# Optimization experiments

Measured on AMD Instinct MI355X. Metric: run time of the kernel, lower is better.

The kernel has to match this reference:

```python
import jax, jax.numpy as jnp
import numpy as np

B, N, D = 4, 4096, 256


def setup_inputs() -> dict:
    key = jax.random.key(0)
    k1, k2 = jax.random.split(key)
    val = jax.random.normal(k1, (B, N, D), dtype=jnp.float32)
    state = jax.random.normal(k2, (B, N), dtype=jnp.float32)
    return {"val": val, "state": state}


def reference(val, state):
    # pairwise_fn: scaled dot-product -> scores [B, N, N]
    scale = val.shape[-1] ** -0.5
    scores = jnp.einsum("bid,bjd->bij", val, val) * scale
    # edge_compress_fn = softsign (non-softmax compression)
    edges = scores / (1.0 + jnp.abs(scores))
    # state_weight_edges=False, val/state projections are Identity
    delta_state = jnp.einsum("bij,bj->bi", edges, state)   # [B, N]
    delta_val = jnp.einsum("bij,bjd->bid", edges, val)      # [B, N, D]
    return (delta_state, delta_val)
```

## Files before the change

### kernel.cpp

```cpp
#include <hip/hip_runtime.h>


#define B_  4
#define N_  4096
#define D_  256

typedef __attribute__((ext_vector_type(8))) short short8;
typedef __attribute__((ext_vector_type(4))) float floatx4;

__device__ __forceinline__ unsigned short f2bf(float f) {
    unsigned int u = __float_as_uint(f);
    u += 0x7fff + ((u >> 16) & 1);
    return (unsigned short)(u >> 16);
}

__device__ __forceinline__ void gl_lds16(const void* g, void* l) {
    __builtin_amdgcn_global_load_lds(
        (const __attribute__((address_space(1))) unsigned int*)g,
        (__attribute__((address_space(3))) unsigned int*)l, 16, 0, 0);
}
__device__ __forceinline__ void gl_lds4(const void* g, void* l) {
    __builtin_amdgcn_global_load_lds(
        (const __attribute__((address_space(1))) unsigned int*)g,
        (__attribute__((address_space(3))) unsigned int*)l, 4, 0, 0);
}

__global__ __launch_bounds__(256)
void prepass_kernel(const float* __restrict__ val,
                    unsigned short* __restrict__ Vb,
                    unsigned short* __restrict__ VF) {
    __shared__ unsigned short tile[64][68];
    const int t   = threadIdx.x;
    const int blk = blockIdx.x;
    const int b   = blk >> 8;
    const int it  = (blk >> 2) & 63;
    const int dt  = blk & 3;
    const int i0  = it * 64, d0 = dt * 64;
    const float*    vb  = val + (size_t)b * N_ * D_;
    unsigned short* Vbb = Vb  + (size_t)b * N_ * D_;
    unsigned short* VFb = VF  + (size_t)b * N_ * D_;

    #pragma unroll
    for (int q = 0; q < 4; ++q) {
        int idx = t + 256 * q;
        int row = idx >> 4;
        int c4  = idx & 15;
        float4 v = *(const float4*)(vb + (size_t)(i0 + row) * D_ + d0 + c4 * 4);
        ushort4 h;
        h.x = f2bf(v.x); h.y = f2bf(v.y); h.z = f2bf(v.z); h.w = f2bf(v.w);
        *(ushort4*)(Vbb + (size_t)(i0 + row) * D_ + d0 + c4 * 4) = h;
        *(ushort4*)&tile[row][c4 * 4] = h;
    }
    __syncthreads();
    #pragma unroll
    for (int q = 0; q < 4; ++q) {
        int dr = (t >> 4) + q * 16;
        int i4 = t & 15;
        ushort4 h;
        h.x = tile[i4 * 4 + 0][dr];
        h.y = tile[i4 * 4 + 1][dr];
        h.z = tile[i4 * 4 + 2][dr];
        h.w = tile[i4 * 4 + 3][dr];
        const int jb = (i0 >> 5) + (i4 >> 3);
        const int e  = (i4 & 7) * 4;
        *(ushort4*)(VFb + ((size_t)jb * 256 + d0 + dr) * 32 + e) = h;
    }
}

__global__ __launch_bounds__(512, 1)
void prop_main(const float* __restrict__ state,
               const unsigned short* __restrict__ Vb,
               const unsigned short* __restrict__ VF,
               float* __restrict__ dvp,
               float* __restrict__ dsp_o)
{
    __shared__ __attribute__((aligned(16))) unsigned char smem[103936];

    const int t    = threadIdx.x;
    const int g    = t >> 8;
    const int w    = t >> 6;
    const int w4   = w & 3;
    const int lane = t & 63;
    const int quad = lane >> 4;
    const int l16  = lane & 15;

    const int x   = blockIdx.x;
    const int it  = x >> 3;
    const int b   = (x >> 1) & 3;
    const int jh  = x & 1;
    const int it0 = it * 128;
    const int jbase = jh * 2048;
    const int niter = 32;

    float* dsredg = (float*)(smem + 102912 + g * 512);

    const unsigned short* Vbb = Vb + (size_t)b * N_ * D_;
    const unsigned short* VFb = VF + (size_t)b * N_ * D_;
    const float*          stb = state + (size_t)b * N_;

    const int hi  = lane >> 5;
    const int p32 = lane & 31;

    int vgoff[4];
    #pragma unroll
    for (int n = 0; n < 4; ++n) {
        int r  = 2 * (w * 4 + n) + hi;
        int gr = p32 ^ (r & 7);
        vgoff[n] = r * 256 + gr * 8;
    }

    const int r0 = (w4 >> 1) * 32;
    const int c0 = (w4 & 1) * 32;
    const int pA = l16 & 7;

    const unsigned short* vf_lane = VFb + (size_t)jh * (64 * 8192)
                                  + w4 * 2048 + l16 * 32 + quad * 8;

    short8 A0[8], A1[8];
    {
        const unsigned short* ar0 = Vbb + (size_t)(it0 + g * 64 + r0 + l16) * 256 + quad * 8;
        const unsigned short* ar1 = ar0 + 16 * 256;
        #pragma unroll
        for (int ks = 0; ks < 8; ++ks) {
            A0[ks] = *(const short8*)(ar0 + ks * 32);
            A1[ks] = *(const short8*)(ar1 + ks * 32);
        }
    }

    #pragma unroll
    for (int n = 0; n < 4; ++n)
        gl_lds16(Vbb + (size_t)jbase * 256 + vgoff[n],
                 smem + (w * 4 + n) * 1024);
    if (w == 0) gl_lds4(stb + jbase + lane, smem + 102400);

    floatx4 dv[4][4];
    #pragma unroll
    for (int a = 0; a < 4; ++a)
        #pragma unroll
        for (int c = 0; c < 4; ++c)
            dv[a][c] = (floatx4){0.f, 0.f, 0.f, 0.f};
    float dsp[8];
    #pragma unroll
    for (int k = 0; k < 8; ++k) dsp[k] = 0.f;

    for (int k = 0; k < niter; ++k) {
        const int buf = k & 1;
        unsigned short* Eshg = (unsigned short*)(smem + 65536 + g * 18432 + buf * 9216);
        unsigned short* vjL  = (unsigned short*)(smem + buf * 32768);
        const float*    stj  = (const float*)(smem + 102400 + buf * 256);

        __syncthreads();

        if (k + 1 < niter) {
            const size_t j0n = jbase + (size_t)(k + 1) * 64;
            #pragma unroll
            for (int n = 0; n < 4; ++n)
                gl_lds16(Vbb + j0n * 256 + vgoff[n],
                         smem + (buf ^ 1) * 32768 + (w * 4 + n) * 1024);
            if (w == 0) gl_lds4(stb + j0n + lane, smem + 102400 + (buf ^ 1) * 256);
        }

        short8 bfr[2][4];
        {
            const unsigned short* vfk = vf_lane + (size_t)k * 16384;
            #pragma unroll
            for (int ks = 0; ks < 2; ++ks)
                #pragma unroll
                for (int c2 = 0; c2 < 4; ++c2)
                    bfr[ks][c2] = *(const short8*)(vfk + ks * 8192 + c2 * 512);
        }

        floatx4 sa[2][2];
        #pragma unroll
        for (int a = 0; a < 2; ++a)
            #pragma unroll
            for (int c = 0; c < 2; ++c)
                sa[a][c] = (floatx4){0.f, 0.f, 0.f, 0.f};

        #pragma unroll
        for (int ks = 0; ks < 8; ++ks) {
            const int p = ((ks * 4 + quad) ^ pA) * 8;
            short8 b0 = *(const short8*)&vjL[(c0 + l16) * 256 + p];
            short8 b1 = *(const short8*)&vjL[(c0 + 16 + l16) * 256 + p];
            sa[0][0] = __builtin_amdgcn_mfma_f32_16x16x32_bf16(A0[ks], b0, sa[0][0], 0, 0, 0);
            sa[0][1] = __builtin_amdgcn_mfma_f32_16x16x32_bf16(A0[ks], b1, sa[0][1], 0, 0, 0);
            sa[1][0] = __builtin_amdgcn_mfma_f32_16x16x32_bf16(A1[ks], b0, sa[1][0], 0, 0, 0);
            sa[1][1] = __builtin_amdgcn_mfma_f32_16x16x32_bf16(A1[ks], b1, sa[1][1], 0, 0, 0);
        }

        float stc0 = stj[c0 + l16];
        float stc1 = stj[c0 + 16 + l16];
        #pragma unroll
        for (int a = 0; a < 2; ++a) {
            #pragma unroll
            for (int r = 0; r < 4; ++r) {
                const int il = r0 + a * 16 + quad * 4 + r;
                float s0 = sa[a][0][r];
                float s1 = sa[a][1][r];
                float e0 = s0 * __builtin_amdgcn_rcpf(16.0f + fabsf(s0));
                float e1 = s1 * __builtin_amdgcn_rcpf(16.0f + fabsf(s1));
                dsp[a * 4 + r] += e0 * stc0 + e1 * stc1;
                Eshg[il * 72 + c0 + l16]      = f2bf(e0);
                Eshg[il * 72 + c0 + 16 + l16] = f2bf(e1);
            }
        }
        __syncthreads();

        #pragma unroll
        for (int ks = 0; ks < 2; ++ks) {
            short8 af[4];
            #pragma unroll
            for (int a2 = 0; a2 < 4; ++a2)
                af[a2] = *(const short8*)&Eshg[(a2 * 16 + l16) * 72 + ks * 32 + quad * 8];
            #pragma unroll
            for (int a2 = 0; a2 < 4; ++a2)
                #pragma unroll
                for (int c2 = 0; c2 < 4; ++c2)
                    dv[a2][c2] = __builtin_amdgcn_mfma_f32_16x16x32_bf16(af[a2], bfr[ks][c2], dv[a2][c2], 0, 0, 0);
        }
    }

    float* dvo = dvp + (size_t)jh * B_ * N_ * D_ + (size_t)b * N_ * D_
                     + (size_t)(it0 + g * 64) * D_;
    #pragma unroll
    for (int a2 = 0; a2 < 4; ++a2)
        #pragma unroll
        for (int c2 = 0; c2 < 4; ++c2)
            #pragma unroll
            for (int r = 0; r < 4; ++r) {
                const int il = a2 * 16 + quad * 4 + r;
                const int d  = w4 * 64 + c2 * 16 + l16;
                dvo[(size_t)il * D_ + d] = dv[a2][c2][r];
            }

    #pragma unroll
    for (int k = 0; k < 8; ++k) {
        float v = dsp[k];
        v += __shfl_xor(v, 1);
        v += __shfl_xor(v, 2);
        v += __shfl_xor(v, 4);
        v += __shfl_xor(v, 8);
        dsp[k] = v;
    }
    if (l16 == 0) {
        #pragma unroll
        for (int a = 0; a < 2; ++a)
            #pragma unroll
            for (int r = 0; r < 4; ++r) {
                const int row = r0 + a * 16 + quad * 4 + r;
                dsredg[(w4 & 1) * 64 + row] = dsp[a * 4 + r];
            }
    }
    __syncthreads();
    if (t < 128) {
        const int gg  = t >> 6;
        const int row = t & 63;
        const float* dsr = (const float*)(smem + 102912 + gg * 512);
        dsp_o[(size_t)jh * B_ * N_ + (size_t)b * N_ + it0 + gg * 64 + row]
            = dsr[row] + dsr[64 + row];
    }
}

__global__ __launch_bounds__(256)
void combine_kernel(const float4* __restrict__ dv0, const float4* __restrict__ dv1,
                    const float*  __restrict__ ds0, const float*  __restrict__ ds1,
                    float* __restrict__ out) {
    const int NDV4 = B_ * N_ * D_ / 4;
    const int NDS  = B_ * N_;
    int x = blockIdx.x * 256 + threadIdx.x;
    if (x < NDV4) {
        float4 a = dv0[x], c = dv1[x];
        float4 r;
        r.x = a.x + c.x; r.y = a.y + c.y; r.z = a.z + c.z; r.w = a.w + c.w;
        ((float4*)(out + NDS))[x] = r;
    } else {
        int y = (x - NDV4) * 4;
        if (y < NDS) {
            float4 a = *(const float4*)(ds0 + y);
            float4 c = *(const float4*)(ds1 + y);
            float4 r;
            r.x = a.x + c.x; r.y = a.y + c.y; r.z = a.z + c.z; r.w = a.w + c.w;
            *(float4*)(out + y) = r;
        }
    }
}

__global__ __launch_bounds__(256, 1)
void prop_kernel_fb(const float* __restrict__ val,
                    const float* __restrict__ state,
                    float* __restrict__ out) {
    __shared__ __attribute__((aligned(16))) unsigned short vi[64][264];
    __shared__ __attribute__((aligned(16))) unsigned short vj[64][264];
    __shared__ __attribute__((aligned(16))) unsigned short vjt[2048][8];
    __shared__ __attribute__((aligned(16))) unsigned short Esh[64][72];
    __shared__ float stj[64];
    __shared__ float dsred[2][64];

    const int t    = threadIdx.x;
    const int w    = t >> 6;
    const int lane = t & 63;
    const int quad = lane >> 4;
    const int l16  = lane & 15;
    const int b   = blockIdx.x >> 6;
    const int it0 = (blockIdx.x & 63) << 6;
    const float* valb = val   + (size_t)b * N_ * D_;
    const float* stb  = state + (size_t)b * N_;

    #pragma unroll
    for (int n = 0; n < 16; ++n) {
        int idx = t + 256 * n;
        int row = idx >> 6;
        int c4  = idx & 63;
        float4 v = *(const float4*)(valb + (size_t)(it0 + row) * D_ + c4 * 4);
        ushort4 h;
        h.x = f2bf(v.x); h.y = f2bf(v.y); h.z = f2bf(v.z); h.w = f2bf(v.w);
        *(ushort4*)&vi[row][c4 * 4] = h;
    }

    const int r0 = (w >> 1) * 32;
    const int c0 = (w & 1) * 32;
    floatx4 dv[4][4];
    #pragma unroll
    for (int a = 0; a < 4; ++a)
        #pragma unroll
        for (int c = 0; c < 4; ++c)
            dv[a][c] = (floatx4){0.f, 0.f, 0.f, 0.f};
    float dsp[8];
    #pragma unroll
    for (int k = 0; k < 8; ++k) dsp[k] = 0.f;

    for (int jt = 0; jt < 64; ++jt) {
        const int j0 = jt * 64;
        #pragma unroll
        for (int n = 0; n < 16; ++n) {
            int idx = t + 256 * n;
            int row = idx >> 6;
            int c4  = idx & 63;
            float4 v = *(const float4*)(valb + (size_t)(j0 + row) * D_ + c4 * 4);
            ushort4 h;
            h.x = f2bf(v.x); h.y = f2bf(v.y); h.z = f2bf(v.z); h.w = f2bf(v.w);
            *(ushort4*)&vj[row][c4 * 4] = h;
        }
        if (t < 64) stj[t] = stb[j0 + t];
        __syncthreads();

        #pragma unroll
        for (int n = 0; n < 8; ++n) {
            const int d  = t;
            const int jb = n;
            short8 pk;
            #pragma unroll
            for (int jj = 0; jj < 8; ++jj) pk[jj] = (short)vj[jb * 8 + jj][d];
            *(short8*)&vjt[d * 8 + (jb ^ (d & 7))][0] = pk;
        }

        floatx4 sa[2][2];
        #pragma unroll
        for (int a = 0; a < 2; ++a)
            #pragma unroll
            for (int c = 0; c < 2; ++c)
                sa[a][c] = (floatx4){0.f, 0.f, 0.f, 0.f};
        #pragma unroll
        for (int ks = 0; ks < 8; ++ks) {
            const int d0 = ks * 32 + quad * 8;
            short8 a0 = *(const short8*)&vi[r0 + l16][d0];
            short8 a1 = *(const short8*)&vi[r0 + 16 + l16][d0];
            short8 b0 = *(const short8*)&vj[c0 + l16][d0];
            short8 b1 = *(const short8*)&vj[c0 + 16 + l16][d0];
            sa[0][0] = __builtin_amdgcn_mfma_f32_16x16x32_bf16(a0, b0, sa[0][0], 0, 0, 0);
            sa[0][1] = __builtin_amdgcn_mfma_f32_16x16x32_bf16(a0, b1, sa[0][1], 0, 0, 0);
            sa[1][0] = __builtin_amdgcn_mfma_f32_16x16x32_bf16(a1, b0, sa[1][0], 0, 0, 0);
            sa[1][1] = __builtin_amdgcn_mfma_f32_16x16x32_bf16(a1, b1, sa[1][1], 0, 0, 0);
        }

        float stc0 = stj[c0 + l16];
        float stc1 = stj[c0 + 16 + l16];
        #pragma unroll
        for (int a = 0; a < 2; ++a) {
            #pragma unroll
            for (int r = 0; r < 4; ++r) {
                const int il = r0 + a * 16 + quad * 4 + r;
                float s0 = sa[a][0][r] * 0.0625f;
                float s1 = sa[a][1][r] * 0.0625f;
                float e0 = s0 / (1.0f + fabsf(s0));
                float e1 = s1 / (1.0f + fabsf(s1));
                dsp[a * 4 + r] += e0 * stc0 + e1 * stc1;
                Esh[il][c0 + l16]      = f2bf(e0);
                Esh[il][c0 + 16 + l16] = f2bf(e1);
            }
        }
        __syncthreads();

        #pragma unroll
        for (int ks = 0; ks < 2; ++ks) {
            short8 af[4], bfr[4];
            #pragma unroll
            for (int a2 = 0; a2 < 4; ++a2)
                af[a2] = *(const short8*)&Esh[a2 * 16 + l16][ks * 32 + quad * 8];
            #pragma unroll
            for (int c2 = 0; c2 < 4; ++c2) {
                const int d  = w * 64 + c2 * 16 + l16;
                const int jb = ks * 4 + quad;
                bfr[c2] = *(const short8*)&vjt[d * 8 + (jb ^ (d & 7))][0];
            }
            #pragma unroll
            for (int a2 = 0; a2 < 4; ++a2)
                #pragma unroll
                for (int c2 = 0; c2 < 4; ++c2)
                    dv[a2][c2] = __builtin_amdgcn_mfma_f32_16x16x32_bf16(af[a2], bfr[c2], dv[a2][c2], 0, 0, 0);
        }
    }

    float* dvo = out + (size_t)B_ * N_ + (size_t)b * N_ * D_;
    #pragma unroll
    for (int a2 = 0; a2 < 4; ++a2)
        #pragma unroll
        for (int c2 = 0; c2 < 4; ++c2)
            #pragma unroll
            for (int r = 0; r < 4; ++r) {
                const int i = it0 + a2 * 16 + quad * 4 + r;
                const int d = w * 64 + c2 * 16 + l16;
                dvo[(size_t)i * D_ + d] = dv[a2][c2][r];
            }

    #pragma unroll
    for (int k = 0; k < 8; ++k) {
        float v = dsp[k];
        v += __shfl_xor(v, 1);
        v += __shfl_xor(v, 2);
        v += __shfl_xor(v, 4);
        v += __shfl_xor(v, 8);
        dsp[k] = v;
    }
    if (l16 == 0) {
        #pragma unroll
        for (int a = 0; a < 2; ++a)
            #pragma unroll
            for (int r = 0; r < 4; ++r) {
                const int row = (w >> 1) * 32 + a * 16 + quad * 4 + r;
                dsred[w & 1][row] = dsp[a * 4 + r];
            }
    }
    __syncthreads();
    if (t < 64) out[(size_t)b * N_ + it0 + t] = dsred[0][t] + dsred[1][t];
}

extern "C" void kernel_launch(void* const* d_in, const int* in_sizes, int n_in,
                              void* d_out, int out_size, void* d_ws, size_t ws_size,
                              hipStream_t stream) {
    const float* val   = (const float*)d_in[0];
    const float* state = (const float*)d_in[1];
    float* out = (float*)d_out;

    const size_t nE         = (size_t)B_ * N_ * D_;
    const size_t need_base  = 2 * nE * sizeof(unsigned short);
    const size_t need_split = need_base + 2 * nE * sizeof(float)
                            + 2 * (size_t)B_ * N_ * sizeof(float);

    if (ws_size >= need_split) {
        unsigned short* Vb = (unsigned short*)d_ws;
        unsigned short* VF = Vb + nE;
        float* dvp = (float*)(VF + nE);
        float* dsp = dvp + 2 * nE;
        prepass_kernel<<<dim3(1024), dim3(256), 0, stream>>>(val, Vb, VF);
        prop_main<<<dim3(256), dim3(512), 0, stream>>>(state, Vb, VF, dvp, dsp);
        const int NDV4 = B_ * N_ * D_ / 4;
        const int NDS4 = B_ * N_ / 4;
        combine_kernel<<<dim3((NDV4 + NDS4) / 256), dim3(256), 0, stream>>>(
            (const float4*)dvp, (const float4*)(dvp + nE),
            dsp, dsp + (size_t)B_ * N_, out);
    } else {
        prop_kernel_fb<<<dim3(256), dim3(256), 0, stream>>>(val, state, out);
    }
}
```

Baseline: 157.7 us.

## Split prop_main blocks into 256-thread 64-row tiles with two blocks per CU

Each block previously held 128 query rows as two 256-thread groups that shared one double-buffered key tile in LDS. Now each block has 256 threads and 64 rows, and twice as many blocks are launched. Launch bounds allow two blocks per CU, so smaller independent blocks can overlap their barriers and memory stalls. The cost is that each key/value tile is loaded from global memory twice as often overall, since it is no longer shared between two row groups.

```diff
diff --git a/kernel.cpp b/kernel.cpp
--- a/kernel.cpp
+++ b/kernel.cpp
@@ -67,19 +67,17 @@
     }
 }
 
-__global__ __launch_bounds__(512, 1)
+__global__ __launch_bounds__(256, 2)
 void prop_main(const float* __restrict__ state,
                const unsigned short* __restrict__ Vb,
                const unsigned short* __restrict__ VF,
                float* __restrict__ dvp,
                float* __restrict__ dsp_o)
 {
-    __shared__ __attribute__((aligned(16))) unsigned char smem[103936];
+    __shared__ __attribute__((aligned(16))) unsigned char smem[75776];
 
     const int t    = threadIdx.x;
-    const int g    = t >> 8;
     const int w    = t >> 6;
-    const int w4   = w & 3;
     const int lane = t & 63;
     const int quad = lane >> 4;
     const int l16  = lane & 15;
@@ -88,11 +86,12 @@
     const int it  = x >> 3;
     const int b   = (x >> 1) & 3;
     const int jh  = x & 1;
-    const int it0 = it * 128;
+    const int it0 = it * 64;
     const int jbase = jh * 2048;
     const int niter = 32;
 
-    float* dsredg = (float*)(smem + 102912 + g * 512);
+    unsigned short* EshL = (unsigned short*)(smem + 65536);
+    float*          dsred = (float*)(smem + 75264);
 
     const unsigned short* Vbb = Vb + (size_t)b * N_ * D_;
     const unsigned short* VFb = VF + (size_t)b * N_ * D_;
@@ -101,24 +100,24 @@
     const int hi  = lane >> 5;
     const int p32 = lane & 31;
 
-    int vgoff[4];
-    #pragma unroll
-    for (int n = 0; n < 4; ++n) {
-        int r  = 2 * (w * 4 + n) + hi;
+    int vgoff[8];
+    #pragma unroll
+    for (int n = 0; n < 8; ++n) {
+        int r  = 2 * (w * 8 + n) + hi;
         int gr = p32 ^ (r & 7);
         vgoff[n] = r * 256 + gr * 8;
     }
 
-    const int r0 = (w4 >> 1) * 32;
-    const int c0 = (w4 & 1) * 32;
+    const int r0 = (w >> 1) * 32;
+    const int c0 = (w & 1) * 32;
     const int pA = l16 & 7;
 
     const unsigned short* vf_lane = VFb + (size_t)jh * (64 * 8192)
-                                  + w4 * 2048 + l16 * 32 + quad * 8;
+                                  + w * 2048 + l16 * 32 + quad * 8;
 
     short8 A0[8], A1[8];
     {
-        const unsigned short* ar0 = Vbb + (size_t)(it0 + g * 64 + r0 + l16) * 256 + quad * 8;
+        const unsigned short* ar0 = Vbb + (size_t)(it0 + r0 + l16) * 256 + quad * 8;
         const unsigned short* ar1 = ar0 + 16 * 256;
         #pragma unroll
         for (int ks = 0; ks < 8; ++ks) {
@@ -128,10 +127,10 @@
     }
 
     #pragma unroll
-    for (int n = 0; n < 4; ++n)
+    for (int n = 0; n < 8; ++n)
         gl_lds16(Vbb + (size_t)jbase * 256 + vgoff[n],
-                 smem + (w * 4 + n) * 1024);
-    if (w == 0) gl_lds4(stb + jbase + lane, smem + 102400);
+                 smem + (w * 8 + n) * 1024);
+    if (w == 0) gl_lds4(stb + jbase + lane, smem + 74752);
 
     floatx4 dv[4][4];
     #pragma unroll
@@ -145,19 +144,18 @@
 
     for (int k = 0; k < niter; ++k) {
         const int buf = k & 1;
-        unsigned short* Eshg = (unsigned short*)(smem + 65536 + g * 18432 + buf * 9216);
-        unsigned short* vjL  = (unsigned short*)(smem + buf * 32768);
-        const float*    stj  = (const float*)(smem + 102400 + buf * 256);
+        unsigned short* vjL = (unsigned short*)(smem + buf * 32768);
+        const float*    stj = (const float*)(smem + 74752 + buf * 256);
 
         __syncthreads();
 
         if (k + 1 < niter) {
             const size_t j0n = jbase + (size_t)(k + 1) * 64;
             #pragma unroll
-            for (int n = 0; n < 4; ++n)
+            for (int n = 0; n < 8; ++n)
                 gl_lds16(Vbb + j0n * 256 + vgoff[n],
-                         smem + (buf ^ 1) * 32768 + (w * 4 + n) * 1024);
-            if (w == 0) gl_lds4(stb + j0n + lane, smem + 102400 + (buf ^ 1) * 256);
+                         smem + (buf ^ 1) * 32768 + (w * 8 + n) * 1024);
+            if (w == 0) gl_lds4(stb + j0n + lane, smem + 74752 + (buf ^ 1) * 256);
         }
 
         short8 bfr[2][4];
@@ -200,8 +198,8 @@
                 float e0 = s0 * __builtin_amdgcn_rcpf(16.0f + fabsf(s0));
                 float e1 = s1 * __builtin_amdgcn_rcpf(16.0f + fabsf(s1));
                 dsp[a * 4 + r] += e0 * stc0 + e1 * stc1;
-                Eshg[il * 72 + c0 + l16]      = f2bf(e0);
-                Eshg[il * 72 + c0 + 16 + l16] = f2bf(e1);
+                EshL[il * 72 + c0 + l16]      = f2bf(e0);
+                EshL[il * 72 + c0 + 16 + l16] = f2bf(e1);
             }
         }
         __syncthreads();
@@ -211,7 +209,7 @@
             short8 af[4];
             #pragma unroll
             for (int a2 = 0; a2 < 4; ++a2)
-                af[a2] = *(const short8*)&Eshg[(a2 * 16 + l16) * 72 + ks * 32 + quad * 8];
+                af[a2] = *(const short8*)&EshL[(a2 * 16 + l16) * 72 + ks * 32 + quad * 8];
             #pragma unroll
             for (int a2 = 0; a2 < 4; ++a2)
                 #pragma unroll
@@ -221,7 +219,7 @@
     }
 
     float* dvo = dvp + (size_t)jh * B_ * N_ * D_ + (size_t)b * N_ * D_
-                     + (size_t)(it0 + g * 64) * D_;
+                     + (size_t)it0 * D_;
     #pragma unroll
     for (int a2 = 0; a2 < 4; ++a2)
         #pragma unroll
@@ -229,7 +227,7 @@
             #pragma unroll
             for (int r = 0; r < 4; ++r) {
                 const int il = a2 * 16 + quad * 4 + r;
-                const int d  = w4 * 64 + c2 * 16 + l16;
+                const int d  = w * 64 + c2 * 16 + l16;
                 dvo[(size_t)il * D_ + d] = dv[a2][c2][r];
             }
 
@@ -248,17 +246,13 @@
             #pragma unroll
             for (int r = 0; r < 4; ++r) {
                 const int row = r0 + a * 16 + quad * 4 + r;
-                dsredg[(w4 & 1) * 64 + row] = dsp[a * 4 + r];
+                dsred[(w & 1) * 64 + row] = dsp[a * 4 + r];
             }
     }
     __syncthreads();
-    if (t < 128) {
-        const int gg  = t >> 6;
-        const int row = t & 63;
-        const float* dsr = (const float*)(smem + 102912 + gg * 512);
-        dsp_o[(size_t)jh * B_ * N_ + (size_t)b * N_ + it0 + gg * 64 + row]
-            = dsr[row] + dsr[64 + row];
-    }
+    if (t < 64)
+        dsp_o[(size_t)jh * B_ * N_ + (size_t)b * N_ + it0 + t]
+            = dsred[t] + dsred[64 + t];
 }
 
 __global__ __launch_bounds__(256)
@@ -463,7 +457,7 @@
         float* dvp = (float*)(VF + nE);
         float* dsp = dvp + 2 * nE;
         prepass_kernel<<<dim3(1024), dim3(256), 0, stream>>>(val, Vb, VF);
-        prop_main<<<dim3(256), dim3(512), 0, stream>>>(state, Vb, VF, dvp, dsp);
+        prop_main<<<dim3(512), dim3(256), 0, stream>>>(state, Vb, VF, dvp, dsp);
         const int NDV4 = B_ * N_ * D_ / 4;
         const int NDS4 = B_ * N_ / 4;
         combine_kernel<<<dim3((NDV4 + NDS4) / 256), dim3(256), 0, stream>>>(
```

Result: faster. 152.0 us (-3.6%).
